# Kernel optimization log

Measured on AMD Instinct MI355X. Metric: run time of the kernel, lower is better.

## Reference

```python
import jax, jax.numpy as jnp
import numpy as np

D = 2048          # hidden_size
I = 8192          # expert_intermediate_size
E = 8             # num_experts
TOP_K = 2
N_CONST = 2       # ConstantExpert count (CONSTANT=2); experts: [copy, zero, ce0, ce1, shared_mlp x (E-4)]


def setup_inputs() -> dict:
    key = jax.random.key(0)
    ks = jax.random.split(key, 9)
    s = 0.02
    return {
        "hidden_states": jax.random.normal(ks[0], (2, 2048, D), dtype=jnp.float32),
        "gate_w1": jax.random.normal(ks[1], (D, E * 8), dtype=jnp.float32) * s,
        "gate_w2": jax.random.normal(ks[2], (E * 8, E), dtype=jnp.float32) * s,
        "ce_wg": jax.random.normal(ks[3], (N_CONST, D, 2), dtype=jnp.float32) * s,
        "ce_const": jax.random.normal(ks[4], (N_CONST, D), dtype=jnp.float32),
        "w_gate": jax.random.normal(ks[5], (D, I), dtype=jnp.float32) * s,
        "w_up": jax.random.normal(ks[6], (D, I), dtype=jnp.float32) * s,
        "w_down": jax.random.normal(ks[7], (I, D), dtype=jnp.float32) * s,
    }


def reference(hidden_states, gate_w1, gate_w2, ce_wg, ce_const, w_gate, w_up, w_down):
    B, S, d = hidden_states.shape
    x = hidden_states.reshape(-1, d).astype(jnp.float32)          # [N, D] tokens

    # Router: MLP gate (fp32) -> softmax -> top-2
    router_logits = jnp.tanh(x @ gate_w1) @ gate_w2               # [N, E]
    probs = jax.nn.softmax(router_logits, axis=-1)
    topw, topi = jax.lax.top_k(probs, TOP_K)                      # [N, 2]
    # mask out last expert (idx == E-1), renormalize
    topw = jnp.where(topi == E - 1, jnp.zeros_like(topw), topw)
    topw = topw / jnp.sum(topw, axis=-1, keepdims=True)
    # per-expert combined routing weight (top-k indices are distinct)
    pe = jnp.sum(topw[..., None] * jax.nn.one_hot(topi, E, dtype=topw.dtype), axis=1)  # [N, E]

    def const_expert(wg, c):
        cw = jax.nn.softmax(x @ wg, axis=-1)                      # [N, 2]
        return cw[:, :1] * x + cw[:, 1:] * c[None, :]

    # shared SwiGLU expert (all dense experts share the same weights in the source)
    swiglu = (jax.nn.silu(x @ w_gate) * (x @ w_up)) @ w_down      # [N, D]

    out = (pe[:, 0:1] * x                                          # CopyExpert (expert 1 = ZeroExpert contributes 0)
           + pe[:, 2:3] * const_expert(ce_wg[0], ce_const[0])
           + pe[:, 3:4] * const_expert(ce_wg[1], ce_const[1])
           + jnp.sum(pe[:, 4:], axis=1, keepdims=True) * swiglu)   # shared dense experts 4..E-1
    return out.reshape(B, S, d), router_logits
```

## Files before the change

### kernel.cpp

```cpp
#include <hip/hip_runtime.h>
#include <stdint.h>
#include <stddef.h>

#define TOKS 4096
#define DH   2048
#define DI   8192

typedef __attribute__((ext_vector_type(8))) short short8v;
typedef __attribute__((ext_vector_type(4))) short short4v;
typedef __attribute__((ext_vector_type(4))) float floatx4;

__device__ __forceinline__ float b2f(short s) {
  union { unsigned u; float f; } v;
  v.u = ((unsigned)(unsigned short)s) << 16;
  return v.f;
}
__device__ __forceinline__ short f2b(float f) {
  union { float f; unsigned u; } v; v.f = f;
  unsigned r = (v.u + 0x7fffu + ((v.u >> 16) & 1u)) >> 16;
  return (short)(unsigned short)r;
}
__device__ __forceinline__ void gload_lds16(const void* g, void* l) {
  __builtin_amdgcn_global_load_lds((const __attribute__((address_space(1))) void*)g,
                                   (__attribute__((address_space(3))) void*)l, 16, 0, 0);
}

__global__ __launch_bounds__(256) void cvt_f32_to_bf16(const float* __restrict__ in,
                                                       short* __restrict__ out) {
  size_t i = (size_t)blockIdx.x * 256 + threadIdx.x;
  floatx4 v = *(const floatx4*)&in[i * 4];
  short4v o;
  o[0] = f2b(v[0]); o[1] = f2b(v[1]); o[2] = f2b(v[2]); o[3] = f2b(v[3]);
  *(short4v*)&out[i * 4] = o;
}

__global__ __launch_bounds__(256) void transpose_to_bf16(const float* __restrict__ in,
                                                         short* __restrict__ out,
                                                         int K, int N,
                                                         int rstride, int roff) {
  __shared__ float tile[32][33];
  const int n0 = blockIdx.x * 32, k0 = blockIdx.y * 32;
  const int tx = threadIdx.x & 31, ty = threadIdx.x >> 5;
#pragma unroll
  for (int yy = 0; yy < 32; yy += 8)
    tile[ty + yy][tx] = in[(size_t)(k0 + ty + yy) * N + n0 + tx];
  __syncthreads();
#pragma unroll
  for (int yy = 0; yy < 32; yy += 8)
    out[((size_t)(n0 + ty + yy) * rstride + roff) * K + k0 + tx] = f2b(tile[tx][ty + yy]);
}

#define RT_TPB 8
__global__ __launch_bounds__(256) void router_kernel(const float* __restrict__ x,
                                                     const float* __restrict__ gw1,
                                                     const float* __restrict__ gw2,
                                                     const float* __restrict__ cwg,
                                                     float* __restrict__ logits_out,
                                                     float* __restrict__ coef) {
  const int wave = threadIdx.x >> 6, lane = threadIdx.x & 63;
  const int tok0 = blockIdx.x * RT_TPB;
  __shared__ float xs[RT_TPB][512];
  __shared__ float ll[RT_TPB][8];
  __shared__ float cd[RT_TPB][4];

  float tj[2] = {0.f, 0.f};
  float cda[2][4] = {{0.f,0.f,0.f,0.f},{0.f,0.f,0.f,0.f}};

  const int st = threadIdx.x >> 5;
  const int sl = threadIdx.x & 31;

  for (int c = 0; c < 4; ++c) {
    const int dbase = c * 512;
#pragma unroll
    for (int r = 0; r < 4; ++r) {
      const int idx = r * 128 + sl * 4;
      *(floatx4*)&xs[st][idx] = *(const floatx4*)&x[(size_t)(tok0 + st) * DH + dbase + idx];
    }
    __syncthreads();
    for (int d = 0; d < 512; ++d) {
      const float g = gw1[(size_t)(dbase + d) * 64 + lane];
      tj[0] += xs[wave * 2 + 0][d] * g;
      tj[1] += xs[wave * 2 + 1][d] * g;
    }
#pragma unroll
    for (int dq = 0; dq < 8; ++dq) {
      const int d = dq * 64 + lane;
      const float w0 = cwg[(size_t)(dbase + d) * 2 + 0];
      const float w1 = cwg[(size_t)(dbase + d) * 2 + 1];
      const float w2 = cwg[(size_t)DH * 2 + (dbase + d) * 2 + 0];
      const float w3 = cwg[(size_t)DH * 2 + (dbase + d) * 2 + 1];
#pragma unroll
      for (int t = 0; t < 2; ++t) {
        const float xv = xs[wave * 2 + t][d];
        cda[t][0] += xv * w0; cda[t][1] += xv * w1;
        cda[t][2] += xv * w2; cda[t][3] += xv * w3;
      }
    }
    __syncthreads();
  }

#pragma unroll
  for (int t = 0; t < 2; ++t) {
    const float th = tanhf(tj[t]);
#pragma unroll
    for (int e = 0; e < 8; ++e) {
      float p = th * gw2[lane * 8 + e];
      for (int off = 32; off; off >>= 1) p += __shfl_xor(p, off);
      if (lane == 0) ll[wave * 2 + t][e] = p;
    }
#pragma unroll
    for (int dd = 0; dd < 4; ++dd) {
      float p = cda[t][dd];
      for (int off = 32; off; off >>= 1) p += __shfl_xor(p, off);
      if (lane == 0) cd[wave * 2 + t][dd] = p;
    }
  }
  __syncthreads();

  if (threadIdx.x < RT_TPB) {
    const int t = threadIdx.x;
    const int gtok = tok0 + t;
    float l[8];
#pragma unroll
    for (int e = 0; e < 8; ++e) l[e] = ll[t][e];
#pragma unroll
    for (int e = 0; e < 8; ++e) logits_out[(size_t)gtok * 8 + e] = l[e];
    float m = l[0];
#pragma unroll
    for (int e = 1; e < 8; ++e) m = fmaxf(m, l[e]);
    float p[8], s = 0.f;
#pragma unroll
    for (int e = 0; e < 8; ++e) { p[e] = expf(l[e] - m); s += p[e]; }
#pragma unroll
    for (int e = 0; e < 8; ++e) p[e] /= s;
    int i1 = 0;
#pragma unroll
    for (int e = 1; e < 8; ++e) if (p[e] > p[i1]) i1 = e;
    int i2 = -1;
#pragma unroll
    for (int e = 0; e < 8; ++e) {
      if (e == i1) continue;
      if (i2 < 0 || p[e] > p[i2]) i2 = e;
    }
    float w1 = (i1 == 7) ? 0.f : p[i1];
    float w2 = (i2 == 7) ? 0.f : p[i2];
    const float nrm = w1 + w2;
    w1 /= nrm; w2 /= nrm;
    float pe[8];
#pragma unroll
    for (int e = 0; e < 8; ++e) pe[e] = 0.f;
    pe[i1] += w1; pe[i2] += w2;
    const float cw00 = 1.f / (1.f + expf(cd[t][1] - cd[t][0]));
    const float cw10 = 1.f / (1.f + expf(cd[t][3] - cd[t][2]));
    coef[gtok * 4 + 0] = pe[0] + pe[2] * cw00 + pe[3] * cw10;
    coef[gtok * 4 + 1] = pe[2] * (1.f - cw00);
    coef[gtok * 4 + 2] = pe[3] * (1.f - cw10);
    coef[gtok * 4 + 3] = pe[4] + pe[5] + pe[6] + pe[7];
  }
}

__device__ __forceinline__ void gemm_mainloop(const short* __restrict__ A,
                                              const short* __restrict__ Bt,
                                              int K, int lda, int ldb,
                                              int m0, int n0,
                                              short* As, short* Bs,
                                              floatx4 (&acc)[4][4]) {
  const int wave = threadIdx.x >> 6;
  const int lane = threadIdx.x & 63;
  const int srow = lane >> 3;
  const int scol = ((lane & 7) ^ srow) * 8;
  const int wm = (wave & 1) * 64;
  const int wn = (wave >> 1) * 64;
  const int l15 = lane & 15;
  const int quad = lane >> 4;
  const int q0 = ((quad ^ (l15 & 7)) * 8);

  for (int k0 = 0; k0 < K; k0 += 64) {
#pragma unroll
    for (int q = 0; q < 4; ++q) {
      const int chunk = wave * 4 + q;
      const int row = chunk * 8 + srow;
      gload_lds16(A + (size_t)(m0 + row) * lda + k0 + scol, &As[chunk * 8 * 64]);
      gload_lds16(Bt + (size_t)(n0 + row) * ldb + k0 + scol, &Bs[chunk * 8 * 64]);
    }
    __syncthreads();
#pragma unroll
    for (int kk = 0; kk < 2; ++kk) {
      const int qo = q0 ^ (kk * 32);
      short8v af[4], bf[4];
#pragma unroll
      for (int i = 0; i < 4; ++i) {
        af[i] = *(const short8v*)&As[(wm + i * 16 + l15) * 64 + qo];
        bf[i] = *(const short8v*)&Bs[(wn + i * 16 + l15) * 64 + qo];
      }
#pragma unroll
      for (int mi = 0; mi < 4; ++mi)
#pragma unroll
        for (int ni = 0; ni < 4; ++ni)
          acc[mi][ni] = __builtin_amdgcn_mfma_f32_16x16x32_bf16(af[mi], bf[ni],
                                                                acc[mi][ni], 0, 0, 0);
    }
    __syncthreads();
  }
}

__global__ __launch_bounds__(256) void gemm1_gu_silu(const short* __restrict__ A,
                                                     const short* __restrict__ Bt,
                                                     short* __restrict__ H,
                                                     int K, int lda, int ldb) {
  __shared__ short As[128 * 64];
  __shared__ short Bs[128 * 64];
  floatx4 acc[4][4];
#pragma unroll
  for (int a = 0; a < 4; ++a)
#pragma unroll
    for (int b = 0; b < 4; ++b) acc[a][b] = (floatx4)0.0f;
  const int lin = blockIdx.y * gridDim.x + blockIdx.x;
  const int m0 = (lin & 31) * 128, n0 = (lin >> 5) * 128;
  gemm_mainloop(A, Bt, K, lda, ldb, m0, n0, As, Bs, acc);
  const int wave = threadIdx.x >> 6, lane = threadIdx.x & 63;
  const int wm = (wave & 1) * 64, wn = (wave >> 1) * 64;
  const int l15 = lane & 15, q4 = (lane >> 4) * 4;
#pragma unroll
  for (int mi = 0; mi < 4; ++mi) {
    const int row0 = m0 + wm + mi * 16 + q4;
#pragma unroll
    for (int ni = 0; ni < 4; ++ni) {
      const int col = n0 + wn + ni * 16 + l15;
#pragma unroll
      for (int rg = 0; rg < 4; ++rg) {
        const float v = acc[mi][ni][rg];
        const float p = __shfl_xor(v, 1);
        if ((l15 & 1) == 0) {
          const float h = (v / (1.f + __expf(-v))) * p;
          H[(size_t)(row0 + rg) * DI + (col >> 1)] = f2b(h);
        }
      }
    }
  }
}

__global__ __launch_bounds__(256) void gemm_bt_moe(const short* __restrict__ A,
                                                   const short* __restrict__ Bt,
                                                   float* __restrict__ out,
                                                   const float* __restrict__ x,
                                                   const float* __restrict__ cc,
                                                   const float* __restrict__ coef,
                                                   int K, int lda, int ldb) {
  __shared__ short As[128 * 64];
  __shared__ short Bs[128 * 64];
  floatx4 acc[4][4];
#pragma unroll
  for (int a = 0; a < 4; ++a)
#pragma unroll
    for (int b = 0; b < 4; ++b) acc[a][b] = (floatx4)0.0f;
  const int lin = blockIdx.y * gridDim.x + blockIdx.x;
  const int m0 = (lin & 31) * 128, n0 = (lin >> 5) * 128;
  gemm_mainloop(A, Bt, K, lda, ldb, m0, n0, As, Bs, acc);
  const int wave = threadIdx.x >> 6, lane = threadIdx.x & 63;
  const int wm = (wave & 1) * 64, wn = (wave >> 1) * 64;
  const int l15 = lane & 15, q4 = (lane >> 4) * 4;
#pragma unroll
  for (int mi = 0; mi < 4; ++mi) {
    const int row0 = m0 + wm + mi * 16 + q4;
#pragma unroll
    for (int ni = 0; ni < 4; ++ni) {
      const int col = n0 + wn + ni * 16 + l15;
      const float c0v = cc[col];
      const float c1v = cc[DH + col];
#pragma unroll
      for (int rg = 0; rg < 4; ++rg) {
        const int row = row0 + rg;
        const floatx4 cf = *(const floatx4*)&coef[row * 4];
        out[(size_t)row * DH + col] =
            cf[0] * x[(size_t)row * DH + col] + cf[1] * c0v + cf[2] * c1v +
            cf[3] * acc[mi][ni][rg];
      }
    }
  }
}

extern "C" void kernel_launch(void* const* d_in, const int* in_sizes, int n_in,
                              void* d_out, int out_size, void* d_ws, size_t ws_size,
                              hipStream_t stream) {
  const float* x   = (const float*)d_in[0];
  const float* gw1 = (const float*)d_in[1];
  const float* gw2 = (const float*)d_in[2];
  const float* cwg = (const float*)d_in[3];
  const float* cc  = (const float*)d_in[4];
  const float* wg  = (const float*)d_in[5];
  const float* wu  = (const float*)d_in[6];
  const float* wd  = (const float*)d_in[7];
  float* out = (float*)d_out;
  float* logits_out = out + (size_t)TOKS * DH;

  char* ws = (char*)d_ws;
  short* xb    = (short*)(ws);
  short* wgwuT = (short*)(ws + 16777216);
  short* wdT   = (short*)(ws + 16777216 + 67108864);
  short* H     = (short*)(ws + 117440512);
  float* coef  = (float*)(ws + 117440512 + 67108864);

  cvt_f32_to_bf16<<<(TOKS * DH) / (256 * 4), 256, 0, stream>>>(x, xb);
  transpose_to_bf16<<<dim3(DI / 32, DH / 32), 256, 0, stream>>>(wg, wgwuT, DH, DI, 2, 0);
  transpose_to_bf16<<<dim3(DI / 32, DH / 32), 256, 0, stream>>>(wu, wgwuT, DH, DI, 2, 1);
  transpose_to_bf16<<<dim3(DH / 32, DI / 32), 256, 0, stream>>>(wd, wdT, DI, DH, 1, 0);
  router_kernel<<<TOKS / RT_TPB, 256, 0, stream>>>(x, gw1, gw2, cwg, logits_out, coef);
  gemm1_gu_silu<<<dim3((2 * DI) / 128, TOKS / 128), 256, 0, stream>>>(
      xb, wgwuT, H, DH, DH, DH);
  gemm_bt_moe<<<dim3(DH / 128, TOKS / 128), 256, 0, stream>>>(
      H, wdT, out, x, cc, coef, DI, DI, DI);
}
```

Measured before the change: 860.1 us.

## Split down-projection GEMM over K into two partials, add combine kernel

The second GEMM (4096x2048 output, K=8192) used only 512 tiles. It is now split along K into two halves written as fp32 partials, which doubles the tile count to 1024 so more CUs are occupied. A separate elementwise kernel sums the partials and applies the MoE combine. The two gate/up weight transposes are merged into one launch via blockIdx.z, and the GEMM dimensions become compile-time constants. The cost is 64MB of extra partial writes and reads plus one more kernel launch.

```diff
diff --git a/kernel.cpp b/kernel.cpp
--- a/kernel.cpp
+++ b/kernel.cpp
@@ -34,20 +34,36 @@
   *(short4v*)&out[i * 4] = o;
 }
 
-__global__ __launch_bounds__(256) void transpose_to_bf16(const float* __restrict__ in,
-                                                         short* __restrict__ out,
-                                                         int K, int N,
-                                                         int rstride, int roff) {
+__global__ __launch_bounds__(256) void transpose_gu(const float* __restrict__ in0,
+                                                    const float* __restrict__ in1,
+                                                    short* __restrict__ out) {
+  const float* in = blockIdx.z ? in1 : in0;
+  const int roff = blockIdx.z;
   __shared__ float tile[32][33];
   const int n0 = blockIdx.x * 32, k0 = blockIdx.y * 32;
   const int tx = threadIdx.x & 31, ty = threadIdx.x >> 5;
 #pragma unroll
   for (int yy = 0; yy < 32; yy += 8)
+    tile[ty + yy][tx] = in[(size_t)(k0 + ty + yy) * DI + n0 + tx];
+  __syncthreads();
+#pragma unroll
+  for (int yy = 0; yy < 32; yy += 8)
+    out[((size_t)(n0 + ty + yy) * 2 + roff) * DH + k0 + tx] = f2b(tile[tx][ty + yy]);
+}
+
+__global__ __launch_bounds__(256) void transpose_to_bf16(const float* __restrict__ in,
+                                                         short* __restrict__ out,
+                                                         int K, int N) {
+  __shared__ float tile[32][33];
+  const int n0 = blockIdx.x * 32, k0 = blockIdx.y * 32;
+  const int tx = threadIdx.x & 31, ty = threadIdx.x >> 5;
+#pragma unroll
+  for (int yy = 0; yy < 32; yy += 8)
     tile[ty + yy][tx] = in[(size_t)(k0 + ty + yy) * N + n0 + tx];
   __syncthreads();
 #pragma unroll
   for (int yy = 0; yy < 32; yy += 8)
-    out[((size_t)(n0 + ty + yy) * rstride + roff) * K + k0 + tx] = f2b(tile[tx][ty + yy]);
+    out[(size_t)(n0 + ty + yy) * K + k0 + tx] = f2b(tile[tx][ty + yy]);
 }
 
 #define RT_TPB 8
@@ -206,8 +222,7 @@
 
 __global__ __launch_bounds__(256) void gemm1_gu_silu(const short* __restrict__ A,
                                                      const short* __restrict__ Bt,
-                                                     short* __restrict__ H,
-                                                     int K, int lda, int ldb) {
+                                                     short* __restrict__ H) {
   __shared__ short As[128 * 64];
   __shared__ short Bs[128 * 64];
   floatx4 acc[4][4];
@@ -217,7 +232,7 @@
     for (int b = 0; b < 4; ++b) acc[a][b] = (floatx4)0.0f;
   const int lin = blockIdx.y * gridDim.x + blockIdx.x;
   const int m0 = (lin & 31) * 128, n0 = (lin >> 5) * 128;
-  gemm_mainloop(A, Bt, K, lda, ldb, m0, n0, As, Bs, acc);
+  gemm_mainloop(A, Bt, DH, DH, DH, m0, n0, As, Bs, acc);
   const int wave = threadIdx.x >> 6, lane = threadIdx.x & 63;
   const int wm = (wave & 1) * 64, wn = (wave >> 1) * 64;
   const int l15 = lane & 15, q4 = (lane >> 4) * 4;
@@ -240,44 +255,56 @@
   }
 }
 
-__global__ __launch_bounds__(256) void gemm_bt_moe(const short* __restrict__ A,
-                                                   const short* __restrict__ Bt,
-                                                   float* __restrict__ out,
+__global__ __launch_bounds__(256) void gemm2_splitk(const short* __restrict__ A,
+                                                    const short* __restrict__ Bt,
+                                                    float* __restrict__ P) {
+  __shared__ short As[128 * 64];
+  __shared__ short Bs[128 * 64];
+  floatx4 acc[4][4];
+#pragma unroll
+  for (int a = 0; a < 4; ++a)
+#pragma unroll
+    for (int b = 0; b < 4; ++b) acc[a][b] = (floatx4)0.0f;
+  const int lin = blockIdx.y * gridDim.x + blockIdx.x;
+  const int m0 = (lin & 31) * 128, n0 = (lin >> 5) * 128;
+  const int kofs = blockIdx.z * (DI / 2);
+  gemm_mainloop(A + kofs, Bt + kofs, DI / 2, DI, DI, m0, n0, As, Bs, acc);
+  float* Pz = P + (size_t)blockIdx.z * TOKS * DH;
+  const int wave = threadIdx.x >> 6, lane = threadIdx.x & 63;
+  const int wm = (wave & 1) * 64, wn = (wave >> 1) * 64;
+  const int l15 = lane & 15, q4 = (lane >> 4) * 4;
+#pragma unroll
+  for (int mi = 0; mi < 4; ++mi) {
+    const int row0 = m0 + wm + mi * 16 + q4;
+#pragma unroll
+    for (int ni = 0; ni < 4; ++ni) {
+      const int col = n0 + wn + ni * 16 + l15;
+#pragma unroll
+      for (int rg = 0; rg < 4; ++rg)
+        Pz[(size_t)(row0 + rg) * DH + col] = acc[mi][ni][rg];
+    }
+  }
+}
+
+__global__ __launch_bounds__(256) void moe_combine(const float* __restrict__ P,
                                                    const float* __restrict__ x,
                                                    const float* __restrict__ cc,
                                                    const float* __restrict__ coef,
-                                                   int K, int lda, int ldb) {
-  __shared__ short As[128 * 64];
-  __shared__ short Bs[128 * 64];
-  floatx4 acc[4][4];
-#pragma unroll
-  for (int a = 0; a < 4; ++a)
-#pragma unroll
-    for (int b = 0; b < 4; ++b) acc[a][b] = (floatx4)0.0f;
-  const int lin = blockIdx.y * gridDim.x + blockIdx.x;
-  const int m0 = (lin & 31) * 128, n0 = (lin >> 5) * 128;
-  gemm_mainloop(A, Bt, K, lda, ldb, m0, n0, As, Bs, acc);
-  const int wave = threadIdx.x >> 6, lane = threadIdx.x & 63;
-  const int wm = (wave & 1) * 64, wn = (wave >> 1) * 64;
-  const int l15 = lane & 15, q4 = (lane >> 4) * 4;
-#pragma unroll
-  for (int mi = 0; mi < 4; ++mi) {
-    const int row0 = m0 + wm + mi * 16 + q4;
-#pragma unroll
-    for (int ni = 0; ni < 4; ++ni) {
-      const int col = n0 + wn + ni * 16 + l15;
-      const float c0v = cc[col];
-      const float c1v = cc[DH + col];
-#pragma unroll
-      for (int rg = 0; rg < 4; ++rg) {
-        const int row = row0 + rg;
-        const floatx4 cf = *(const floatx4*)&coef[row * 4];
-        out[(size_t)row * DH + col] =
-            cf[0] * x[(size_t)row * DH + col] + cf[1] * c0v + cf[2] * c1v +
-            cf[3] * acc[mi][ni][rg];
-      }
-    }
-  }
+                                                   float* __restrict__ out) {
+  const size_t i = ((size_t)blockIdx.x * 256 + threadIdx.x) * 4;
+  const int row = (int)(i >> 11);
+  const int col = (int)(i & 2047);
+  const floatx4 p0 = *(const floatx4*)&P[i];
+  const floatx4 p1 = *(const floatx4*)&P[(size_t)TOKS * DH + i];
+  const floatx4 xv = *(const floatx4*)&x[i];
+  const floatx4 c0 = *(const floatx4*)&cc[col];
+  const floatx4 c1 = *(const floatx4*)&cc[DH + col];
+  const floatx4 cf = *(const floatx4*)&coef[row * 4];
+  floatx4 o;
+#pragma unroll
+  for (int e = 0; e < 4; ++e)
+    o[e] = cf[0] * xv[e] + cf[1] * c0[e] + cf[2] * c1[e] + cf[3] * (p0[e] + p1[e]);
+  *(floatx4*)&out[i] = o;
 }
 
 extern "C" void kernel_launch(void* const* d_in, const int* in_sizes, int n_in,
@@ -299,15 +326,14 @@
   short* wgwuT = (short*)(ws + 16777216);
   short* wdT   = (short*)(ws + 16777216 + 67108864);
   short* H     = (short*)(ws + 117440512);
-  float* coef  = (float*)(ws + 117440512 + 67108864);
+  float* P     = (float*)(ws + 117440512 + 67108864);
+  float* coef  = (float*)(ws + 117440512 + 67108864 + 67108864);
 
   cvt_f32_to_bf16<<<(TOKS * DH) / (256 * 4), 256, 0, stream>>>(x, xb);
-  transpose_to_bf16<<<dim3(DI / 32, DH / 32), 256, 0, stream>>>(wg, wgwuT, DH, DI, 2, 0);
-  transpose_to_bf16<<<dim3(DI / 32, DH / 32), 256, 0, stream>>>(wu, wgwuT, DH, DI, 2, 1);
-  transpose_to_bf16<<<dim3(DH / 32, DI / 32), 256, 0, stream>>>(wd, wdT, DI, DH, 1, 0);
+  transpose_gu<<<dim3(DI / 32, DH / 32, 2), 256, 0, stream>>>(wg, wu, wgwuT);
+  transpose_to_bf16<<<dim3(DH / 32, DI / 32), 256, 0, stream>>>(wd, wdT, DI, DH);
   router_kernel<<<TOKS / RT_TPB, 256, 0, stream>>>(x, gw1, gw2, cwg, logits_out, coef);
-  gemm1_gu_silu<<<dim3((2 * DI) / 128, TOKS / 128), 256, 0, stream>>>(
-      xb, wgwuT, H, DH, DH, DH);
-  gemm_bt_moe<<<dim3(DH / 128, TOKS / 128), 256, 0, stream>>>(
-      H, wdT, out, x, cc, coef, DI, DI, DI);
-}
+  gemm1_gu_silu<<<dim3((2 * DI) / 128, TOKS / 128), 256, 0, stream>>>(xb, wgwuT, H);
+  gemm2_splitk<<<dim3(DH / 128, TOKS / 128, 2), 256, 0, stream>>>(H, wdT, P);
+  moe_combine<<<(TOKS * DH) / (256 * 4), 256, 0, stream>>>(P, x, cc, coef, out);
+}
```

Result: slower. 957.1 us (+11.3%).
